# Kernel tuning notes

Hardware: AMD Instinct MI355X
Metric: run time of the kernel (lower is better)

The kernel has to match this reference:

```python
import jax, jax.numpy as jnp
import numpy as np

DIM = 256
MEM = 2048
N = 65536

def setup_inputs() -> dict:
    key = jax.random.key(0)
    ks = jax.random.split(key, 8)
    features = jax.random.normal(ks[0], (N, DIM), dtype=jnp.float32)
    coords = jax.random.uniform(ks[1], (N, 2), dtype=jnp.float32)
    memory = jax.random.normal(ks[2], (MEM, DIM), dtype=jnp.float32)
    # pos_mlp: Linear(2, dim) -> ReLU -> Linear(dim, dim); torch Linear: y = x @ W.T + b
    w1 = jax.random.normal(ks[3], (DIM, 2), dtype=jnp.float32) / jnp.sqrt(2.0)
    b1 = jax.random.normal(ks[4], (DIM,), dtype=jnp.float32) * 0.01
    w2 = jax.random.normal(ks[5], (DIM, DIM), dtype=jnp.float32) / jnp.sqrt(DIM * 1.0)
    b2 = jax.random.normal(ks[6], (DIM,), dtype=jnp.float32) * 0.01
    return {"features": features, "coords": coords, "memory": memory,
            "w1": w1, "b1": b1, "w2": w2, "b2": b2}

def reference(features, coords, memory, w1, b1, w2, b2):
    # tiny pos MLP on the mean coordinate -> [1, dim]
    mean_xy = jnp.mean(coords, axis=0, keepdims=True)            # [1, 2]
    h = jax.nn.relu(mean_xy @ w1.T + b1)                         # [1, dim]
    spatial_emb = h @ w2.T + b2                                  # [1, dim]
    z = features + spatial_emb                                   # [N, dim]
    scale = 1.0 / jnp.sqrt(jnp.asarray(features.shape[-1], features.dtype))
    scores = (z @ memory.T) * scale                              # [N, mem]
    attn = jax.nn.softmax(scores, axis=-1)
    return attn @ memory                                         # [N, dim]
```

## Files before the change

### kernel.cpp

```cpp
#include <hip/hip_runtime.h>
#include <hip/hip_bf16.h>

#define DIM 256
#define MEMN 2048
#define NROWS 65536
#define KVB 32
#define NT 64
#define TILE_B 32768

typedef __bf16 bf16x8 __attribute__((ext_vector_type(8)));
typedef float f32x4 __attribute__((ext_vector_type(4)));
typedef float f32x16 __attribute__((ext_vector_type(16)));
typedef unsigned int uint32x4 __attribute__((ext_vector_type(4)));

__global__ void prep_coords_kernel(const float* __restrict__ coords,
                                   float* __restrict__ partial) {
    __shared__ float red[512];
    int b = blockIdx.x, t = threadIdx.x;
    const f32x4* src = reinterpret_cast<const f32x4*>(coords + (size_t)b * 2048);
    f32x4 v0 = src[t * 2];
    f32x4 v1 = src[t * 2 + 1];
    red[t]       = v0[0] + v0[2] + v1[0] + v1[2];
    red[256 + t] = v0[1] + v0[3] + v1[1] + v1[3];
    __syncthreads();
    for (int s = 128; s > 0; s >>= 1) {
        if (t < s) { red[t] += red[t + s]; red[256 + t] += red[256 + t + s]; }
        __syncthreads();
    }
    if (t == 0) { partial[b] = red[0]; partial[64 + b] = red[256]; }
}

__global__ void prep_emb_kernel(const float* __restrict__ partial,
                                const float* __restrict__ w1,
                                const float* __restrict__ b1,
                                const float* __restrict__ w2,
                                const float* __restrict__ b2,
                                float* __restrict__ emb) {
    __shared__ float red[128];
    __shared__ float h[DIM];
    int t = threadIdx.x;
    if (t < 128) red[t] = partial[t];
    __syncthreads();
    for (int s = 32; s > 0; s >>= 1) {
        if (t < s) { red[t] += red[t + s]; red[64 + t] += red[64 + t + s]; }
        __syncthreads();
    }
    float mx = red[0] * (1.0f / NROWS);
    float my = red[64] * (1.0f / NROWS);
    float hv = mx * w1[2 * t] + my * w1[2 * t + 1] + b1[t];
    h[t] = hv > 0.f ? hv : 0.f;
    __syncthreads();
    float acc = b2[t];
    const float* wr = w2 + (size_t)t * DIM;
    #pragma unroll 4
    for (int k = 0; k < DIM; k += 4) {
        f32x4 wv = *reinterpret_cast<const f32x4*>(wr + k);
        acc += h[k] * wv[0] + h[k + 1] * wv[1] + h[k + 2] * wv[2] + h[k + 3] * wv[3];
    }
    emb[t] = acc;
}

__global__ void prep_blob_kernel(const float* __restrict__ mem,
                                 __bf16* __restrict__ blob) {
    __shared__ __bf16 ltile[KVB][DIM];
    int tile = blockIdx.x, t = threadIdx.x;
    int kt = tile * KVB;
    for (int c = t; c < 1024; c += 256) {
        int e = c * 8, row = e >> 8, col = e & 255;
        const float* s = mem + (size_t)(kt + row) * DIM + col;
        f32x4 a = *reinterpret_cast<const f32x4*>(s);
        f32x4 b = *reinterpret_cast<const f32x4*>(s + 4);
        bf16x8 o;
        #pragma unroll
        for (int j = 0; j < 4; ++j) { o[j] = (__bf16)a[j]; o[j + 4] = (__bf16)b[j]; }
        *reinterpret_cast<bf16x8*>(&ltile[row][col]) = o;
    }
    __syncthreads();
    __bf16* kb = blob + (size_t)tile * 16384;
    __bf16* vb = kb + 8192;
    for (int c = t; c < 1024; c += 256) {
        int e = c * 8, kv = e >> 8, x0 = e & 255;
        bf16x8 o = *reinterpret_cast<const bf16x8*>(&ltile[kv][x0 ^ (kv << 3)]);
        *reinterpret_cast<bf16x8*>(kb + e) = o;
    }
    for (int c = t; c < 1024; c += 256) {
        int idx = c * 8, R = idx >> 7, j0 = idx & 127;
        int L0 = j0 ^ ((R & 15) << 3);
        int d = 4 * R + (L0 >> 5), kv0 = L0 & 31;
        bf16x8 o;
        #pragma unroll
        for (int j = 0; j < 8; ++j) o[j] = ltile[kv0 + j][d];
        *reinterpret_cast<bf16x8*>(vb + idx) = o;
    }
}

__device__ __forceinline__ void gload_lds16(const void* g, void* l) {
    __builtin_amdgcn_global_load_lds(
        (const __attribute__((address_space(1))) unsigned int*)g,
        (__attribute__((address_space(3))) unsigned int*)l,
        16, 0, 0);
}

__device__ __forceinline__ unsigned int pkbf(float a, float b) {
    union { __bf16 h; unsigned short u; } ua, ub;
    ua.h = (__bf16)a; ub.h = (__bf16)b;
    return (unsigned int)ua.u | ((unsigned int)ub.u << 16);
}

__global__ __launch_bounds__(256, 2)
void flash_kernel(const float* __restrict__ feat,
                  const float* __restrict__ emb,
                  const __bf16* __restrict__ blob,
                  float* __restrict__ out) {
    __shared__ char smem[2 * TILE_B];

    const int t = threadIdx.x;
    const int w = t >> 6;
    const int lane = t & 63;
    const int ln = lane & 31;
    const int hi = lane >> 5;

    const int qrow = blockIdx.x * 128 + w * 32 + ln;

    bf16x8 qf[16];
    {
        const float* frow = feat + (size_t)qrow * DIM;
        #pragma unroll
        for (int kd = 0; kd < 16; ++kd) {
            int d0 = kd * 16 + hi * 8;
            f32x4 a = *reinterpret_cast<const f32x4*>(frow + d0);
            f32x4 b = *reinterpret_cast<const f32x4*>(frow + d0 + 4);
            f32x4 ea = *reinterpret_cast<const f32x4*>(emb + d0);
            f32x4 eb = *reinterpret_cast<const f32x4*>(emb + d0 + 4);
            bf16x8 q;
            #pragma unroll
            for (int i = 0; i < 4; ++i) {
                q[i]     = (__bf16)((a[i] + ea[i]) * 0.0625f);
                q[i + 4] = (__bf16)((b[i] + eb[i]) * 0.0625f);
            }
            qf[kd] = q;
        }
    }

    f32x16 o[8];
    #pragma unroll
    for (int dt = 0; dt < 8; ++dt) o[dt] = (f32x16)(0.f);
    float m = -1e30f, l = 0.f;

    const char* gsl = (const char*)blob + w * 8192 + lane * 16;
    char* bA = smem;
    char* bB = smem + TILE_B;

    #define STAGE(k, buf)                                            \
        {   const char* _g = gsl + (size_t)(k) * TILE_B;             \
            char* _d = (buf) + w * 8192;                             \
            _Pragma("unroll")                                        \
            for (int _j = 0; _j < 8; ++_j)                           \
                gload_lds16(_g + _j * 1024, _d + _j * 1024);         \
        }

    #define QKT(buf, dst)                                                        \
        {   f32x16 _acc = (f32x16)(0.f);                                         \
            const char* _kb = (buf) + ln * 512;                                  \
            __builtin_amdgcn_s_setprio(1);                                       \
            _Pragma("unroll")                                                    \
            for (int _kd = 0; _kd < 16; ++_kd) {                                 \
                const bf16x8 _a = *reinterpret_cast<const bf16x8*>(              \
                    _kb + (((_kd * 16 + hi * 8) ^ (ln * 8)) << 1));              \
                _acc = __builtin_amdgcn_mfma_f32_32x32x16_bf16(_a, qf[_kd], _acc, 0, 0, 0); \
            }                                                                    \
            __builtin_amdgcn_s_setprio(0);                                       \
            (dst) = _acc;                                                        \
        }

    STAGE(0, bA);
    asm volatile("s_waitcnt vmcnt(0)" ::: "memory");
    __builtin_amdgcn_s_barrier();
    asm volatile("" ::: "memory");
    f32x16 s_cur, s_nxt;
    QKT(bA, s_cur);

    #pragma unroll 1
    for (int kt = 0; kt < NT; ++kt) {
        if (kt + 1 < NT) STAGE(kt + 1, bB);

        float pmax = -1e30f;
        #pragma unroll
        for (int e = 0; e < 16; ++e) pmax = fmaxf(pmax, s_cur[e]);
        pmax = fmaxf(pmax, __shfl_xor(pmax, 32));
        if (pmax > m + 8.f) {
            float sc = __expf(m - pmax);
            m = pmax;
            l *= sc;
            #pragma unroll
            for (int dt = 0; dt < 8; ++dt) o[dt] = o[dt] * sc;
        }
        f32x16 p;
        float ladd = 0.f;
        #pragma unroll
        for (int e = 0; e < 16; ++e) {
            float pe = __expf(s_cur[e] - m);
            p[e] = pe;
            ladd += pe;
        }
        ladd += __shfl_xor(ladd, 32);
        l += ladd;

        #pragma unroll
        for (int ks = 0; ks < 2; ++ks) {
            unsigned w01 = pkbf(p[ks * 8 + 0], p[ks * 8 + 1]);
            unsigned w23 = pkbf(p[ks * 8 + 2], p[ks * 8 + 3]);
            unsigned w45 = pkbf(p[ks * 8 + 4], p[ks * 8 + 5]);
            unsigned w67 = pkbf(p[ks * 8 + 6], p[ks * 8 + 7]);
            unsigned sA = hi ? w01 : w45;
            unsigned sB = hi ? w23 : w67;
            unsigned oA = hi ? w45 : w01;
            unsigned oB = hi ? w67 : w23;
            unsigned rA = __shfl_xor(sA, 32);
            unsigned rB = __shfl_xor(sB, 32);
            uint32x4 fw;
            fw[0] = hi ? rA : oA;
            fw[1] = hi ? rB : oB;
            fw[2] = hi ? oA : rA;
            fw[3] = hi ? oB : rB;
            bf16x8 pb = __builtin_bit_cast(bf16x8, fw);
            const int kv0 = ks * 16 + hi * 8;
            __builtin_amdgcn_s_setprio(1);
            #pragma unroll
            for (int dt = 0; dt < 8; ++dt) {
                int R = dt * 8 + (ln >> 2);
                int j = (((ln & 3) * 32 + kv0) ^ ((R & 15) << 3));
                const bf16x8 va = *reinterpret_cast<const bf16x8*>(
                    bA + 16384 + R * 256 + 2 * j);
                o[dt] = __builtin_amdgcn_mfma_f32_32x32x16_bf16(va, pb, o[dt], 0, 0, 0);
            }
            __builtin_amdgcn_s_setprio(0);
        }

        if (kt + 1 < NT) {
            asm volatile("s_waitcnt vmcnt(0)" ::: "memory");
            __builtin_amdgcn_s_barrier();
            asm volatile("" ::: "memory");
            QKT(bB, s_nxt);
            char* tmp = bA; bA = bB; bB = tmp;
            s_cur = s_nxt;
        }
    }

    float linv = 1.f / l;
    __syncthreads();
    #pragma unroll 1
    for (int ph = 0; ph < 2; ++ph) {
        if ((w >> 1) == ph) {
            char* base = smem + ((w & 1) * 32 + ln) * 1024;
            const int sw = (ln & 7) << 4;
            #pragma unroll
            for (int dt = 0; dt < 8; ++dt) {
                #pragma unroll
                for (int g = 0; g < 4; ++g) {
                    f32x4 v;
                    v[0] = o[dt][4 * g + 0] * linv;
                    v[1] = o[dt][4 * g + 1] * linv;
                    v[2] = o[dt][4 * g + 2] * linv;
                    v[3] = o[dt][4 * g + 3] * linv;
                    *reinterpret_cast<f32x4*>(base + ((dt * 128 + g * 32 + hi * 16) ^ sw)) = v;
                }
            }
        }
        __syncthreads();
        {
            char* gdst = (char*)out + ((size_t)blockIdx.x * 128 + ph * 64) * 1024;
            #pragma unroll
            for (int i = 0; i < 16; ++i) {
                int bo = t * 16 + i * 4096;
                int r = bo >> 10, off = bo & 1023;
                f32x4 v = *reinterpret_cast<const f32x4*>(
                    smem + r * 1024 + (off ^ ((r & 7) << 4)));
                *reinterpret_cast<f32x4*>(gdst + (size_t)r * 1024 + off) = v;
            }
        }
        __syncthreads();
    }
    #undef STAGE
    #undef QKT
}

extern "C" void kernel_launch(void* const* d_in, const int* in_sizes, int n_in,
                              void* d_out, int out_size, void* d_ws, size_t ws_size,
                              hipStream_t stream) {
    const float* features = (const float*)d_in[0];
    const float* coords   = (const float*)d_in[1];
    const float* memory   = (const float*)d_in[2];
    const float* w1       = (const float*)d_in[3];
    const float* b1       = (const float*)d_in[4];
    const float* w2       = (const float*)d_in[5];
    const float* b2       = (const float*)d_in[6];
    float* out = (float*)d_out;

    float*  partial = (float*)d_ws;
    float*  emb     = (float*)((char*)d_ws + 512);
    __bf16* blob    = (__bf16*)((char*)d_ws + 2048);

    prep_coords_kernel<<<64, 256, 0, stream>>>(coords, partial);
    prep_blob_kernel<<<NT, 256, 0, stream>>>(memory, blob);
    prep_emb_kernel<<<1, 256, 0, stream>>>(partial, w1, b1, w2, b2, emb);
    flash_kernel<<<NROWS / 128, 256, 0, stream>>>(features, emb, blob, out);
}
```

Measured before the change: 206.2 us.

## Software-pipeline QK^T of next tile with PV of current tile, use exp2

Restructures the flash-attention main loop so the QK^T MFMAs for tile k+1 are interleaved with the PV MFMAs for tile k, and softmax runs between barriers while the next tile is staged. QK^T is split into two independent accumulators to shorten the MFMA dependency chain. The query scale now folds in log2(e) so exp2 replaces exp, and the rescale test becomes wave-uniform via __any with a wider threshold. This adds register pressure (extra score accumulators and packed P fragments) and reorders barriers, which could lower occupancy or cause spills.

```diff
diff --git a/kernel.cpp b/kernel.cpp
--- a/kernel.cpp
+++ b/kernel.cpp
@@ -107,6 +107,14 @@
     return (unsigned int)ua.u | ((unsigned int)ub.u << 16);
 }
 
+__device__ __forceinline__ float fexp2(float x) {
+#if __has_builtin(__builtin_amdgcn_exp2f)
+    return __builtin_amdgcn_exp2f(x);
+#else
+    return exp2f(x);
+#endif
+}
+
 __global__ __launch_bounds__(256, 2)
 void flash_kernel(const float* __restrict__ feat,
                   const float* __restrict__ emb,
@@ -122,6 +130,7 @@
 
     const int qrow = blockIdx.x * 128 + w * 32 + ln;
 
+    const float QS = 0.0901684463f;
     bf16x8 qf[16];
     {
         const float* frow = feat + (size_t)qrow * DIM;
@@ -135,8 +144,8 @@
             bf16x8 q;
             #pragma unroll
             for (int i = 0; i < 4; ++i) {
-                q[i]     = (__bf16)((a[i] + ea[i]) * 0.0625f);
-                q[i + 4] = (__bf16)((b[i] + eb[i]) * 0.0625f);
+                q[i]     = (__bf16)((a[i] + ea[i]) * QS);
+                q[i + 4] = (__bf16)((b[i] + eb[i]) * QS);
             }
             qf[kd] = q;
         }
@@ -150,6 +159,9 @@
     const char* gsl = (const char*)blob + w * 8192 + lane * 16;
     char* bA = smem;
     char* bB = smem + TILE_B;
+
+    f32x16 sa, sb;
+    bf16x8 pb0, pb1;
 
     #define STAGE(k, buf)                                            \
         {   const char* _g = gsl + (size_t)(k) * TILE_B;             \
@@ -159,93 +171,114 @@
                 gload_lds16(_g + _j * 1024, _d + _j * 1024);         \
         }
 
-    #define QKT(buf, dst)                                                        \
-        {   f32x16 _acc = (f32x16)(0.f);                                         \
-            const char* _kb = (buf) + ln * 512;                                  \
-            __builtin_amdgcn_s_setprio(1);                                       \
+    #define KFRAG(buf, kd) \
+        (*reinterpret_cast<const bf16x8*>((buf) + ln * 512 + ((((kd) * 16 + hi * 8) ^ (ln * 8)) << 1)))
+
+    #define VFRAG(buf, dt, ks)                                                   \
+        (*reinterpret_cast<const bf16x8*>((buf) + 16384 +                        \
+            ((dt) * 8 + (ln >> 2)) * 256 +                                       \
+            (((((ln & 3) * 32 + (ks) * 16 + hi * 8)) ^ ((((dt) * 8 + (ln >> 2)) & 15) << 3)) << 1)))
+
+    #define SOFTMAX()                                                            \
+        {   f32x16 _s;                                                           \
             _Pragma("unroll")                                                    \
-            for (int _kd = 0; _kd < 16; ++_kd) {                                 \
-                const bf16x8 _a = *reinterpret_cast<const bf16x8*>(              \
-                    _kb + (((_kd * 16 + hi * 8) ^ (ln * 8)) << 1));              \
-                _acc = __builtin_amdgcn_mfma_f32_32x32x16_bf16(_a, qf[_kd], _acc, 0, 0, 0); \
+            for (int _e = 0; _e < 16; ++_e) _s[_e] = sa[_e] + sb[_e];            \
+            float _pm = fmaxf(_s[0], _s[1]);                                     \
+            _Pragma("unroll")                                                    \
+            for (int _e = 2; _e < 16; ++_e) _pm = fmaxf(_pm, _s[_e]);            \
+            _pm = fmaxf(_pm, __shfl_xor(_pm, 32));                               \
+            if (__any(_pm > m + 11.5f)) {                                        \
+                float _mn = fmaxf(m, _pm);                                       \
+                float _sc = fexp2(m - _mn);                                      \
+                m = _mn;                                                         \
+                l *= _sc;                                                        \
+                _Pragma("unroll")                                                \
+                for (int _dt = 0; _dt < 8; ++_dt) o[_dt] = o[_dt] * _sc;         \
             }                                                                    \
-            __builtin_amdgcn_s_setprio(0);                                       \
-            (dst) = _acc;                                                        \
+            float _la = 0.f;                                                     \
+            _Pragma("unroll")                                                    \
+            for (int _e = 0; _e < 16; ++_e) {                                    \
+                float _p = fexp2(_s[_e] - m);                                    \
+                _s[_e] = _p;                                                     \
+                _la += _p;                                                       \
+            }                                                                    \
+            _la += __shfl_xor(_la, 32);                                          \
+            l += _la;                                                            \
+            _Pragma("unroll")                                                    \
+            for (int _ks = 0; _ks < 2; ++_ks) {                                  \
+                unsigned _w01 = pkbf(_s[_ks * 8 + 0], _s[_ks * 8 + 1]);          \
+                unsigned _w23 = pkbf(_s[_ks * 8 + 2], _s[_ks * 8 + 3]);          \
+                unsigned _w45 = pkbf(_s[_ks * 8 + 4], _s[_ks * 8 + 5]);          \
+                unsigned _w67 = pkbf(_s[_ks * 8 + 6], _s[_ks * 8 + 7]);          \
+                unsigned _sA = hi ? _w01 : _w45;                                 \
+                unsigned _sB = hi ? _w23 : _w67;                                 \
+                unsigned _oA = hi ? _w45 : _w01;                                 \
+                unsigned _oB = hi ? _w67 : _w23;                                 \
+                unsigned _rA = __shfl_xor(_sA, 32);                              \
+                unsigned _rB = __shfl_xor(_sB, 32);                              \
+                uint32x4 _fw;                                                    \
+                _fw[0] = hi ? _rA : _oA;                                         \
+                _fw[1] = hi ? _rB : _oB;                                         \
+                _fw[2] = hi ? _oA : _rA;                                         \
+                _fw[3] = hi ? _oB : _rB;                                         \
+                if (_ks == 0) pb0 = __builtin_bit_cast(bf16x8, _fw);             \
+                else          pb1 = __builtin_bit_cast(bf16x8, _fw);             \
+            }                                                                    \
         }
 
     STAGE(0, bA);
     asm volatile("s_waitcnt vmcnt(0)" ::: "memory");
     __builtin_amdgcn_s_barrier();
     asm volatile("" ::: "memory");
-    f32x16 s_cur, s_nxt;
-    QKT(bA, s_cur);
+    sa = (f32x16)(0.f);
+    sb = (f32x16)(0.f);
+    __builtin_amdgcn_s_setprio(1);
+    #pragma unroll
+    for (int i = 0; i < 8; ++i) {
+        sa = __builtin_amdgcn_mfma_f32_32x32x16_bf16(KFRAG(bA, 2 * i),     qf[2 * i],     sa, 0, 0, 0);
+        sb = __builtin_amdgcn_mfma_f32_32x32x16_bf16(KFRAG(bA, 2 * i + 1), qf[2 * i + 1], sb, 0, 0, 0);
+    }
+    __builtin_amdgcn_s_setprio(0);
+    STAGE(1, bB);
+    SOFTMAX();
+    asm volatile("s_waitcnt vmcnt(0)" ::: "memory");
+    __builtin_amdgcn_s_barrier();
+    asm volatile("" ::: "memory");
 
     #pragma unroll 1
-    for (int kt = 0; kt < NT; ++kt) {
-        if (kt + 1 < NT) STAGE(kt + 1, bB);
-
-        float pmax = -1e30f;
+    for (int kt = 0; kt < NT - 1; ++kt) {
+        sa = (f32x16)(0.f);
+        sb = (f32x16)(0.f);
+        __builtin_amdgcn_s_setprio(1);
         #pragma unroll
-        for (int e = 0; e < 16; ++e) pmax = fmaxf(pmax, s_cur[e]);
-        pmax = fmaxf(pmax, __shfl_xor(pmax, 32));
-        if (pmax > m + 8.f) {
-            float sc = __expf(m - pmax);
-            m = pmax;
-            l *= sc;
-            #pragma unroll
-            for (int dt = 0; dt < 8; ++dt) o[dt] = o[dt] * sc;
-        }
-        f32x16 p;
-        float ladd = 0.f;
-        #pragma unroll
-        for (int e = 0; e < 16; ++e) {
-            float pe = __expf(s_cur[e] - m);
-            p[e] = pe;
-            ladd += pe;
-        }
-        ladd += __shfl_xor(ladd, 32);
-        l += ladd;
-
-        #pragma unroll
-        for (int ks = 0; ks < 2; ++ks) {
-            unsigned w01 = pkbf(p[ks * 8 + 0], p[ks * 8 + 1]);
-            unsigned w23 = pkbf(p[ks * 8 + 2], p[ks * 8 + 3]);
-            unsigned w45 = pkbf(p[ks * 8 + 4], p[ks * 8 + 5]);
-            unsigned w67 = pkbf(p[ks * 8 + 6], p[ks * 8 + 7]);
-            unsigned sA = hi ? w01 : w45;
-            unsigned sB = hi ? w23 : w67;
-            unsigned oA = hi ? w45 : w01;
-            unsigned oB = hi ? w67 : w23;
-            unsigned rA = __shfl_xor(sA, 32);
-            unsigned rB = __shfl_xor(sB, 32);
-            uint32x4 fw;
-            fw[0] = hi ? rA : oA;
-            fw[1] = hi ? rB : oB;
-            fw[2] = hi ? oA : rA;
-            fw[3] = hi ? oB : rB;
-            bf16x8 pb = __builtin_bit_cast(bf16x8, fw);
-            const int kv0 = ks * 16 + hi * 8;
-            __builtin_amdgcn_s_setprio(1);
-            #pragma unroll
-            for (int dt = 0; dt < 8; ++dt) {
-                int R = dt * 8 + (ln >> 2);
-                int j = (((ln & 3) * 32 + kv0) ^ ((R & 15) << 3));
-                const bf16x8 va = *reinterpret_cast<const bf16x8*>(
-                    bA + 16384 + R * 256 + 2 * j);
-                o[dt] = __builtin_amdgcn_mfma_f32_32x32x16_bf16(va, pb, o[dt], 0, 0, 0);
-            }
-            __builtin_amdgcn_s_setprio(0);
-        }
-
-        if (kt + 1 < NT) {
-            asm volatile("s_waitcnt vmcnt(0)" ::: "memory");
-            __builtin_amdgcn_s_barrier();
-            asm volatile("" ::: "memory");
-            QKT(bB, s_nxt);
-            char* tmp = bA; bA = bB; bB = tmp;
-            s_cur = s_nxt;
-        }
-    }
+        for (int i = 0; i < 8; ++i) {
+            sa = __builtin_amdgcn_mfma_f32_32x32x16_bf16(KFRAG(bB, 2 * i),     qf[2 * i],     sa, 0, 0, 0);
+            o[i] = __builtin_amdgcn_mfma_f32_32x32x16_bf16(VFRAG(bA, i, 0), pb0, o[i], 0, 0, 0);
+            sb = __builtin_amdgcn_mfma_f32_32x32x16_bf16(KFRAG(bB, 2 * i + 1), qf[2 * i + 1], sb, 0, 0, 0);
+            o[i] = __builtin_amdgcn_mfma_f32_32x32x16_bf16(VFRAG(bA, i, 1), pb1, o[i], 0, 0, 0);
+        }
+        __builtin_amdgcn_s_setprio(0);
+
+        asm volatile("" ::: "memory");
+        __builtin_amdgcn_s_barrier();
+        asm volatile("" ::: "memory");
+
+        if (kt + 2 < NT) STAGE(kt + 2, bA);
+        SOFTMAX();
+        asm volatile("s_waitcnt vmcnt(0)" ::: "memory");
+        __builtin_amdgcn_s_barrier();
+        asm volatile("" ::: "memory");
+
+        char* tmp = bA; bA = bB; bB = tmp;
+    }
+
+    __builtin_amdgcn_s_setprio(1);
+    #pragma unroll
+    for (int i = 0; i < 8; ++i) {
+        o[i] = __builtin_amdgcn_mfma_f32_32x32x16_bf16(VFRAG(bA, i, 0), pb0, o[i], 0, 0, 0);
+        o[i] = __builtin_amdgcn_mfma_f32_32x32x16_bf16(VFRAG(bA, i, 1), pb1, o[i], 0, 0, 0);
+    }
+    __builtin_amdgcn_s_setprio(0);
 
     float linv = 1.f / l;
     __syncthreads();
@@ -282,7 +315,9 @@
         __syncthreads();
     }
     #undef STAGE
-    #undef QKT
+    #undef KFRAG
+    #undef VFRAG
+    #undef SOFTMAX
 }
 
 extern "C" void kernel_launch(void* const* d_in, const int* in_sizes, int n_in,
```

Result: faster. 192.3 us (-6.7%).
